# Optimization experiments

Hardware: AMD Instinct MI355X
Metric: run time of the kernel (lower is better)

## Reference

```python
import jax, jax.numpy as jnp
import numpy as np

RANK, N, T, S = 8, 64, 64, 64
IN_F, OUT_F = N * T, N * S  # 4096, 4096


def setup_inputs() -> dict:
    key = jax.random.key(0)
    k1, k2, k3, k4 = jax.random.split(key, 4)
    scale = 1.0 / np.sqrt(IN_F)
    x = jax.random.normal(k1, (8, 2048, IN_F), dtype=jnp.float32)
    A = jax.random.normal(k2, (RANK, N, T), dtype=jnp.float32) * scale
    B = jax.random.normal(k3, (RANK, S, N), dtype=jnp.float32) * scale
    bias = jax.random.uniform(k4, (OUT_F,), dtype=jnp.float32, minval=-scale, maxval=scale)
    return {"x": x, "A": A, "B": B, "bias": bias}


def reference(x, A, B, bias):
    # Kronecker-product weight reconstruction: sum over rank b of
    # W[i*S+k, j*N+m] = sum_b A[b,i,j] * B[b,k,m]
    W = jnp.einsum('bij,bkm->ikjm', A, B).reshape(OUT_F, IN_F)
    # F.linear: x @ W.T + bias
    return jnp.einsum('bsi,oi->bso', x, W) + bias
```

## Files before the change

kernel.cpp:

```cpp
#include <hip/hip_runtime.h>
#include <hip/hip_bf16.h>
#include <stdint.h>

#define M_DIM 16384
#define N_DIM 4096
#define K_DIM 4096

typedef short short8 __attribute__((ext_vector_type(8)));
typedef unsigned short ushort8 __attribute__((ext_vector_type(8)));
typedef float f32x4 __attribute__((ext_vector_type(4)));

__device__ __forceinline__ unsigned short f2b(float f) {
    union { float f; uint32_t u; } v; v.f = f;
    return (unsigned short)((v.u + 0x7FFFu + ((v.u >> 16) & 1u)) >> 16);
}

__device__ __forceinline__ void async_ld16(const void* g, void* l) {
    __builtin_amdgcn_global_load_lds(
        (const __attribute__((address_space(1))) uint32_t*)g,
        (__attribute__((address_space(3))) uint32_t*)l, 16, 0, 0);
}

__global__ __launch_bounds__(256) void build_w_kernel(
    const float* __restrict__ A, const float* __restrict__ B,
    unsigned short* __restrict__ W)
{
    size_t idx = ((size_t)blockIdx.x * 256 + threadIdx.x) * 8;
    int o = (int)(idx >> 12);
    int c = (int)(idx & 4095);
    int i = o >> 6, k = o & 63;
    int j = c >> 6, m0 = c & 63;

    float acc[8];
#pragma unroll
    for (int t = 0; t < 8; ++t) acc[t] = 0.0f;
#pragma unroll
    for (int b = 0; b < 8; ++b) {
        float a = A[b * 4096 + i * 64 + j];
        const float4* bp = (const float4*)&B[b * 4096 + k * 64 + m0];
        float4 b0 = bp[0], b1 = bp[1];
        acc[0] += a * b0.x; acc[1] += a * b0.y;
        acc[2] += a * b0.z; acc[3] += a * b0.w;
        acc[4] += a * b1.x; acc[5] += a * b1.y;
        acc[6] += a * b1.z; acc[7] += a * b1.w;
    }
    ushort8 r;
#pragma unroll
    for (int t = 0; t < 8; ++t) r[t] = f2b(acc[t]);
    *(ushort8*)&W[idx] = r;
}

__global__ __launch_bounds__(256) void cvt_x_kernel(
    const float* __restrict__ x, unsigned short* __restrict__ xb)
{
    size_t idx = ((size_t)blockIdx.x * 256 + threadIdx.x) * 8;
    const float4* gp = (const float4*)&x[idx];
    float4 v0 = gp[0], v1 = gp[1];
    ushort8 r;
    r[0] = f2b(v0.x); r[1] = f2b(v0.y); r[2] = f2b(v0.z); r[3] = f2b(v0.w);
    r[4] = f2b(v1.x); r[5] = f2b(v1.y); r[6] = f2b(v1.z); r[7] = f2b(v1.w);
    *(ushort8*)&xb[idx] = r;
}

template <bool PRECONV>
__global__ __launch_bounds__(256, 2) void gemm_kernel(
    const float* __restrict__ xf,
    const unsigned short* __restrict__ xb,
    const unsigned short* __restrict__ W,
    const float* __restrict__ bias,
    float* __restrict__ out)
{
    __shared__ unsigned short As[128 * 32];
    __shared__ unsigned short Bs[128 * 32];

    const int tid = threadIdx.x;
    const int wave = tid >> 6;
    const int lane = tid & 63;
    const int quad = lane >> 4;
    const int l15 = lane & 15;
    const int wm = (wave >> 1) * 64;
    const int wn = (wave & 1) * 64;
    const size_t mbase = (size_t)blockIdx.y * 128;
    const int nbase = blockIdx.x * 128;

    f32x4 acc[4][4];
#pragma unroll
    for (int a = 0; a < 4; ++a)
#pragma unroll
        for (int b = 0; b < 4; ++b)
            acc[a][b] = (f32x4){0.0f, 0.0f, 0.0f, 0.0f};

    for (int k0 = 0; k0 < K_DIM; k0 += 32) {
        {
            const int issue0 = wave * 2;
#pragma unroll
            for (int t = 0; t < 2; ++t) {
                const int isn = issue0 + t;
                const int row = isn * 16 + (lane >> 2);
                const int kc = (lane & 3) * 8;
                async_ld16(&W[(size_t)(nbase + row) * K_DIM + k0 + kc],
                           &Bs[isn * 512]);
            }
        }
        if (PRECONV) {
            const int issue0 = wave * 2;
#pragma unroll
            for (int t = 0; t < 2; ++t) {
                const int isn = issue0 + t;
                const int row = isn * 16 + (lane >> 2);
                const int kc = (lane & 3) * 8;
                async_ld16(&xb[(mbase + row) * K_DIM + k0 + kc],
                           &As[isn * 512]);
            }
        } else {
            const int row = tid >> 1;
            const int half = tid & 1;
            const float* gp = xf + (mbase + row) * K_DIM + k0 + half * 16;
            float4 v0 = ((const float4*)gp)[0];
            float4 v1 = ((const float4*)gp)[1];
            float4 v2 = ((const float4*)gp)[2];
            float4 v3 = ((const float4*)gp)[3];
            ushort8 lo, hi;
            lo[0] = f2b(v0.x); lo[1] = f2b(v0.y); lo[2] = f2b(v0.z); lo[3] = f2b(v0.w);
            lo[4] = f2b(v1.x); lo[5] = f2b(v1.y); lo[6] = f2b(v1.z); lo[7] = f2b(v1.w);
            hi[0] = f2b(v2.x); hi[1] = f2b(v2.y); hi[2] = f2b(v2.z); hi[3] = f2b(v2.w);
            hi[4] = f2b(v3.x); hi[5] = f2b(v3.y); hi[6] = f2b(v3.z); hi[7] = f2b(v3.w);
            *(ushort8*)&As[row * 32 + half * 16] = lo;
            *(ushort8*)&As[row * 32 + half * 16 + 8] = hi;
        }
        __syncthreads();

        short8 af[4], bf[4];
#pragma unroll
        for (int mt = 0; mt < 4; ++mt)
            af[mt] = *(const short8*)&As[(wm + mt * 16 + l15) * 32 + quad * 8];
#pragma unroll
        for (int nt = 0; nt < 4; ++nt)
            bf[nt] = *(const short8*)&Bs[(wn + nt * 16 + l15) * 32 + quad * 8];
#pragma unroll
        for (int mt = 0; mt < 4; ++mt)
#pragma unroll
            for (int nt = 0; nt < 4; ++nt)
                acc[mt][nt] = __builtin_amdgcn_mfma_f32_16x16x32_bf16(
                    af[mt], bf[nt], acc[mt][nt], 0, 0, 0);
        __syncthreads();
    }

    float bv[4];
#pragma unroll
    for (int nt = 0; nt < 4; ++nt) bv[nt] = bias[nbase + wn + nt * 16 + l15];
#pragma unroll
    for (int mt = 0; mt < 4; ++mt) {
#pragma unroll
        for (int r = 0; r < 4; ++r) {
            const size_t row = mbase + wm + mt * 16 + quad * 4 + r;
            float* orow = out + row * N_DIM + nbase + wn + l15;
#pragma unroll
            for (int nt = 0; nt < 4; ++nt)
                orow[nt * 16] = acc[mt][nt][r] + bv[nt];
        }
    }
}

extern "C" void kernel_launch(void* const* d_in, const int* in_sizes, int n_in,
                              void* d_out, int out_size, void* d_ws, size_t ws_size,
                              hipStream_t stream)
{
    const float* x = (const float*)d_in[0];
    const float* A = (const float*)d_in[1];
    const float* B = (const float*)d_in[2];
    const float* bias = (const float*)d_in[3];
    float* out = (float*)d_out;

    unsigned short* Wb = (unsigned short*)d_ws;
    const size_t wbytes = (size_t)N_DIM * K_DIM * 2;
    const size_t xbytes = (size_t)M_DIM * K_DIM * 2;

    build_w_kernel<<<(N_DIM * (size_t)K_DIM) / 8 / 256, 256, 0, stream>>>(A, B, Wb);

    if (ws_size >= wbytes + xbytes) {
        unsigned short* xbuf = (unsigned short*)((char*)d_ws + wbytes);
        cvt_x_kernel<<<((size_t)M_DIM * K_DIM) / 8 / 256, 256, 0, stream>>>(x, xbuf);
        gemm_kernel<true><<<dim3(N_DIM / 128, M_DIM / 128), 256, 0, stream>>>(
            nullptr, xbuf, Wb, bias, out);
    } else {
        gemm_kernel<false><<<dim3(N_DIM / 128, M_DIM / 128), 256, 0, stream>>>(
            x, nullptr, Wb, bias, out);
    }
}
```

Measured before the change: 1.063 ms.

## Fuse fp32-to-bf16 conversion of x into GEMM and swizzle LDS to avoid bank conflicts

Removes the separate x conversion kernel and the bf16 copy of x in workspace. The GEMM now loads fp32 x directly and converts it in registers using a cheaper round-half-up packing. The A tile in LDS is padded to a stride of 40, and the W tile uses an XOR swizzle on the async-load source column and the fragment read, both to cut bank conflicts. The cost is reading fp32 x (twice the bytes) once per N-block tile, with the synchronous conversion left unoverlapped. The rounding also changes from round-to-nearest-even to round-half-up.

```diff
diff --git a/kernel.cpp b/kernel.cpp
--- a/kernel.cpp
+++ b/kernel.cpp
@@ -9,10 +9,15 @@
 typedef short short8 __attribute__((ext_vector_type(8)));
 typedef unsigned short ushort8 __attribute__((ext_vector_type(8)));
 typedef float f32x4 __attribute__((ext_vector_type(4)));
+typedef uint32_t u32x4 __attribute__((ext_vector_type(4)));
 
 __device__ __forceinline__ unsigned short f2b(float f) {
     union { float f; uint32_t u; } v; v.f = f;
     return (unsigned short)((v.u + 0x7FFFu + ((v.u >> 16) & 1u)) >> 16);
+}
+
+__device__ __forceinline__ uint32_t pk_bf16(uint32_t a, uint32_t b) {
+    return ((a + 0x8000u) >> 16) | ((b + 0x8000u) & 0xFFFF0000u);
 }
 
 __device__ __forceinline__ void async_ld16(const void* g, void* l) {
@@ -50,28 +55,16 @@
     *(ushort8*)&W[idx] = r;
 }
 
-__global__ __launch_bounds__(256) void cvt_x_kernel(
-    const float* __restrict__ x, unsigned short* __restrict__ xb)
-{
-    size_t idx = ((size_t)blockIdx.x * 256 + threadIdx.x) * 8;
-    const float4* gp = (const float4*)&x[idx];
-    float4 v0 = gp[0], v1 = gp[1];
-    ushort8 r;
-    r[0] = f2b(v0.x); r[1] = f2b(v0.y); r[2] = f2b(v0.z); r[3] = f2b(v0.w);
-    r[4] = f2b(v1.x); r[5] = f2b(v1.y); r[6] = f2b(v1.z); r[7] = f2b(v1.w);
-    *(ushort8*)&xb[idx] = r;
-}
+#define AS_STRIDE 40
 
-template <bool PRECONV>
 __global__ __launch_bounds__(256, 2) void gemm_kernel(
     const float* __restrict__ xf,
-    const unsigned short* __restrict__ xb,
     const unsigned short* __restrict__ W,
     const float* __restrict__ bias,
     float* __restrict__ out)
 {
-    __shared__ unsigned short As[128 * 32];
-    __shared__ unsigned short Bs[128 * 32];
+    __shared__ __align__(16) unsigned short As[128 * AS_STRIDE];
+    __shared__ __align__(16) unsigned short Bs[128 * 32];
 
     const int tid = threadIdx.x;
     const int wave = tid >> 6;
@@ -83,6 +76,12 @@
     const size_t mbase = (size_t)blockIdx.y * 128;
     const int nbase = blockIdx.x * 128;
 
+    const int brow_in_issue = lane >> 2;
+    const int c_g = (lane & 3) ^ ((lane >> 3) & 3);
+    const int arow = tid >> 1;
+    const int ahalf = tid & 1;
+    const float* aptr = xf + (mbase + arow) * K_DIM + ahalf * 16;
+
     f32x4 acc[4][4];
 #pragma unroll
     for (int a = 0; a < 4; ++a)
@@ -91,52 +90,40 @@
             acc[a][b] = (f32x4){0.0f, 0.0f, 0.0f, 0.0f};
 
     for (int k0 = 0; k0 < K_DIM; k0 += 32) {
+#pragma unroll
+        for (int t = 0; t < 2; ++t) {
+            const int isn = wave * 2 + t;
+            const int row = isn * 16 + brow_in_issue;
+            async_ld16(&W[(size_t)(nbase + row) * K_DIM + k0 + c_g * 8],
+                       &Bs[isn * 512]);
+        }
         {
-            const int issue0 = wave * 2;
-#pragma unroll
-            for (int t = 0; t < 2; ++t) {
-                const int isn = issue0 + t;
-                const int row = isn * 16 + (lane >> 2);
-                const int kc = (lane & 3) * 8;
-                async_ld16(&W[(size_t)(nbase + row) * K_DIM + k0 + kc],
-                           &Bs[isn * 512]);
-            }
-        }
-        if (PRECONV) {
-            const int issue0 = wave * 2;
-#pragma unroll
-            for (int t = 0; t < 2; ++t) {
-                const int isn = issue0 + t;
-                const int row = isn * 16 + (lane >> 2);
-                const int kc = (lane & 3) * 8;
-                async_ld16(&xb[(mbase + row) * K_DIM + k0 + kc],
-                           &As[isn * 512]);
-            }
-        } else {
-            const int row = tid >> 1;
-            const int half = tid & 1;
-            const float* gp = xf + (mbase + row) * K_DIM + k0 + half * 16;
-            float4 v0 = ((const float4*)gp)[0];
-            float4 v1 = ((const float4*)gp)[1];
-            float4 v2 = ((const float4*)gp)[2];
-            float4 v3 = ((const float4*)gp)[3];
-            ushort8 lo, hi;
-            lo[0] = f2b(v0.x); lo[1] = f2b(v0.y); lo[2] = f2b(v0.z); lo[3] = f2b(v0.w);
-            lo[4] = f2b(v1.x); lo[5] = f2b(v1.y); lo[6] = f2b(v1.z); lo[7] = f2b(v1.w);
-            hi[0] = f2b(v2.x); hi[1] = f2b(v2.y); hi[2] = f2b(v2.z); hi[3] = f2b(v2.w);
-            hi[4] = f2b(v3.x); hi[5] = f2b(v3.y); hi[6] = f2b(v3.z); hi[7] = f2b(v3.w);
-            *(ushort8*)&As[row * 32 + half * 16] = lo;
-            *(ushort8*)&As[row * 32 + half * 16 + 8] = hi;
+            const uint32_t* gp = (const uint32_t*)(aptr + k0);
+            u32x4 v0 = ((const u32x4*)gp)[0];
+            u32x4 v1 = ((const u32x4*)gp)[1];
+            u32x4 v2 = ((const u32x4*)gp)[2];
+            u32x4 v3 = ((const u32x4*)gp)[3];
+            u32x4 lo, hi;
+            lo[0] = pk_bf16(v0[0], v0[1]); lo[1] = pk_bf16(v0[2], v0[3]);
+            lo[2] = pk_bf16(v1[0], v1[1]); lo[3] = pk_bf16(v1[2], v1[3]);
+            hi[0] = pk_bf16(v2[0], v2[1]); hi[1] = pk_bf16(v2[2], v2[3]);
+            hi[2] = pk_bf16(v3[0], v3[1]); hi[3] = pk_bf16(v3[2], v3[3]);
+            uint32_t* wp = (uint32_t*)&As[arow * AS_STRIDE + ahalf * 16];
+            *(u32x4*)wp = lo;
+            *(u32x4*)(wp + 4) = hi;
         }
         __syncthreads();
 
         short8 af[4], bf[4];
 #pragma unroll
         for (int mt = 0; mt < 4; ++mt)
-            af[mt] = *(const short8*)&As[(wm + mt * 16 + l15) * 32 + quad * 8];
+            af[mt] = *(const short8*)&As[(wm + mt * 16 + l15) * AS_STRIDE + quad * 8];
 #pragma unroll
-        for (int nt = 0; nt < 4; ++nt)
-            bf[nt] = *(const short8*)&Bs[(wn + nt * 16 + l15) * 32 + quad * 8];
+        for (int nt = 0; nt < 4; ++nt) {
+            const int row = wn + nt * 16 + l15;
+            const int pchunk = quad ^ ((row >> 1) & 3);
+            bf[nt] = *(const short8*)&Bs[row * 32 + pchunk * 8];
+        }
 #pragma unroll
         for (int mt = 0; mt < 4; ++mt)
 #pragma unroll
@@ -173,18 +160,8 @@
     float* out = (float*)d_out;
 
     unsigned short* Wb = (unsigned short*)d_ws;
-    const size_t wbytes = (size_t)N_DIM * K_DIM * 2;
-    const size_t xbytes = (size_t)M_DIM * K_DIM * 2;
 
     build_w_kernel<<<(N_DIM * (size_t)K_DIM) / 8 / 256, 256, 0, stream>>>(A, B, Wb);
-
-    if (ws_size >= wbytes + xbytes) {
-        unsigned short* xbuf = (unsigned short*)((char*)d_ws + wbytes);
-        cvt_x_kernel<<<((size_t)M_DIM * K_DIM) / 8 / 256, 256, 0, stream>>>(x, xbuf);
-        gemm_kernel<true><<<dim3(N_DIM / 128, M_DIM / 128), 256, 0, stream>>>(
-            nullptr, xbuf, Wb, bias, out);
-    } else {
-        gemm_kernel<false><<<dim3(N_DIM / 128, M_DIM / 128), 256, 0, stream>>>(
-            x, nullptr, Wb, bias, out);
-    }
+    gemm_kernel<<<dim3(N_DIM / 128, M_DIM / 128), 256, 0, stream>>>(
+        x, Wb, bias, out);
 }
```

New measurement: 1.251 ms. 17.7% more time.
